# Optimization experiments

Measured on AMD Instinct MI355X. Metric: run time of the kernel, lower is better.

Reference implementation:

```python
import jax, jax.numpy as jnp
import numpy as np

EPS = 1e-6


def _conv(x, w, b=None, pad=0, groups=1):
    out = jax.lax.conv_general_dilated(
        x, w, window_strides=(1, 1), padding=[(pad, pad), (pad, pad)],
        feature_group_count=groups,
        dimension_numbers=("NCHW", "OIHW", "NCHW"))
    if b is not None:
        out = out + b[None, :, None, None]
    return out


def _win_patches(t):
    # t: [B, C, H, W] -> [B, C, 25, H, W]; 5x5 zero-padded sliding windows
    # (equivalent to torch nn.Unfold(5, padding=2), grouped per channel)
    B, C, H, W = t.shape
    p = jax.lax.conv_general_dilated_patches(
        t.reshape(B * C, 1, H, W), filter_shape=(5, 5),
        window_strides=(1, 1), padding=[(2, 2), (2, 2)])
    return p.reshape(B, C, 25, H, W)


def _gradient_consistency(gx, gy):
    mag = jnp.sqrt(gx * gx + gy * gy + EPS)
    direction = jnp.arctan2(gy, gx)
    dp = _win_patches(direction)          # [B,C,25,H,W]
    mp = _win_patches(mag)                # [B,C,25,H,W]
    sum_m = mp.sum(axis=2)                # [B,C,H,W]
    wmean = (dp * mp).sum(axis=2) / (sum_m + EPS)
    wvar = ((dp - wmean[:, :, None]) ** 2 * mp).sum(axis=2) / (sum_m + EPS)
    wstd = jnp.sqrt(wvar)
    return 1.0 - jnp.tanh(wstd)           # [B,C,H,W]


def setup_inputs() -> dict:
    key = jax.random.key(0)
    B, C, H, W = 2, 64, 128, 128
    C4 = C // 4
    ks = jax.random.split(key, 12)
    s = 0.02
    sobel_x = jnp.array([[-1, 0, 1], [-2, 0, 2], [-1, 0, 1]], jnp.float32)
    sobel_y = jnp.array([[-1, -2, -1], [0, 0, 0], [1, 2, 1]], jnp.float32)
    return {
        "x": jax.random.normal(ks[0], (B, C, H, W), jnp.float32),
        "w_gx": jnp.tile(sobel_x[None, None], (C, 1, 1, 1)),
        "w_gy": jnp.tile(sobel_y[None, None], (C, 1, 1, 1)),
        "ga_w1": jax.random.normal(ks[1], (C, 2 * C, 1, 1), jnp.float32) * s,
        "ga_b1": jnp.zeros((C,), jnp.float32),
        "ga_w2": jax.random.normal(ks[2], (C4, C, 1, 1), jnp.float32) * s,
        "ga_b2": jnp.zeros((C4,), jnp.float32),
        "cd_w1": jax.random.normal(ks[3], (C4, C4, 3, 3), jnp.float32) * s,
        "cd_b1": jnp.zeros((C4,), jnp.float32),
        "cd_w2": jax.random.normal(ks[4], (1, C4, 1, 1), jnp.float32) * s,
        "cd_b2": jnp.zeros((1,), jnp.float32),
        "ec_w1": jax.random.normal(ks[5], (C, C, 3, 3), jnp.float32) * s,
        "ec_b1": jnp.zeros((C,), jnp.float32),
        "ec_w2": jax.random.normal(ks[6], (C, C, 3, 3), jnp.float32) * s,
        "ec_b2": jnp.zeros((C,), jnp.float32),
        "alpha": jnp.float32(0.1),
    }


def reference(x, w_gx, w_gy, ga_w1, ga_b1, ga_w2, ga_b2,
              cd_w1, cd_b1, cd_w2, cd_b2,
              ec_w1, ec_b1, ec_w2, ec_b2, alpha):
    C = x.shape[1]
    # Sobel depthwise gradients
    gx = _conv(x, w_gx, pad=1, groups=C)
    gy = _conv(x, w_gy, pad=1, groups=C)
    # gradient analyzer (1x1 convs)
    gf = jnp.concatenate([gx, gy], axis=1)
    ga = jax.nn.relu(_conv(gf, ga_w1, ga_b1))
    ga = jax.nn.relu(_conv(ga, ga_w2, ga_b2))
    # windowed weighted direction stats
    consistency = _gradient_consistency(gx, gy)
    # consistency detector
    ew = jax.nn.relu(_conv(ga, cd_w1, cd_b1, pad=1))
    ew = jax.nn.sigmoid(_conv(ew, cd_w2, cd_b2))        # [B,1,H,W]
    ew = ew * consistency.mean(axis=1, keepdims=True)
    # edge branch
    ee = jax.nn.relu(_conv(x, ec_w1, ec_b1, pad=1))
    ee = _conv(ee, ec_w2, ec_b2, pad=1)
    return x + alpha * ew * ee
```

## Files before the change

kernel.cpp:

```cpp
#include <hip/hip_runtime.h>
#include <math.h>

#define Hd 128
#define Wd 128
#define HW 16384
#define EPSc 1e-6f

typedef __attribute__((ext_vector_type(8))) short s8v;
typedef __attribute__((ext_vector_type(4))) float f4v;

__device__ __forceinline__ unsigned short f2bf(float f) {
    unsigned int u = __float_as_uint(f);
    unsigned int r = (u + 0x7FFFu + ((u >> 16) & 1u)) >> 16;
    return (unsigned short)r;
}

__global__ void k_prepxh(const float* __restrict__ x,
                         const float* __restrict__ ga_w1, const float* __restrict__ ga_w2,
                         const float* __restrict__ cd_w1,
                         const float* __restrict__ ec_w1, const float* __restrict__ ec_w2,
                         unsigned short* __restrict__ xh,
                         unsigned short* __restrict__ w1m, unsigned short* __restrict__ w2m,
                         float* __restrict__ cd_w1t,
                         unsigned short* __restrict__ w1h, unsigned short* __restrict__ w2h,
                         float* __restrict__ cm) {
    int bid = blockIdx.x;
    if (bid < 128) {
        int p = bid * 256 + threadIdx.x;
        int b = p >> 14, s = p & (HW - 1);
        const float* xp = x + (size_t)b * 64 * HW + s;
        alignas(16) unsigned short buf[64];
#pragma unroll
        for (int c = 0; c < 64; c++) buf[c] = f2bf(xp[c * HW]);
        uint4* dst = (uint4*)(xh + (size_t)p * 64);
        const uint4* src = (const uint4*)buf;
#pragma unroll
        for (int i = 0; i < 8; i++) dst[i] = src[i];
        return;
    }
    int i = (bid - 128) * 256 + threadIdx.x;
    if (i < 36864) {
        int t = i >> 12, co = (i >> 6) & 63, ci = i & 63;
        w1h[i] = f2bf(ec_w1[(co * 64 + ci) * 9 + t]);
    } else if (i < 73728) {
        int j = i - 36864;
        int t = j >> 12, co = (j >> 6) & 63, ci = j & 63;
        w2h[j] = f2bf(ec_w2[(co * 64 + ci) * 9 + t]);
    } else if (i < 81920) {
        int j = i - 73728;
        w1m[j] = f2bf(ga_w1[j]);
    } else if (i < 82944) {
        int j = i - 81920;
        w2m[j] = f2bf(ga_w2[j]);
    } else if (i < 85248) {
        int j = i - 82944;
        int co = j & 15, r = j >> 4, t = r % 9, ci = r / 9;
        cd_w1t[j] = cd_w1[(co * 16 + ci) * 9 + t];
    } else if (i < 118016) {
        cm[i - 85248] = 0.f;
    }
}

__global__ __launch_bounds__(256, 8)
void k_sobcons(const float* __restrict__ x,
               const float* __restrict__ wgx, const float* __restrict__ wgy,
               unsigned short* __restrict__ gxgyh,
               float* __restrict__ cm) {
    __shared__ float xt[484];
    __shared__ float lm[480];
    __shared__ float ld[480];
    int tid = threadIdx.x;
    int tx = tid & 15, ty = tid >> 4;
    int x0 = blockIdx.x * 16, y0 = blockIdx.y * 16;
    int b = blockIdx.z >> 4, cb = (blockIdx.z & 15) * 4;
    float acc = 0.f;
    for (int c = 0; c < 4; c++) {
        int ch = cb + c;
        const float* xp = x + (size_t)(b * 64 + ch) * HW;
        float wx[9], wy[9];
#pragma unroll
        for (int i = 0; i < 9; i++) { wx[i] = wgx[ch * 9 + i]; wy[i] = wgy[ch * 9 + i]; }
        __syncthreads();
        for (int i = tid; i < 484; i += 256) {
            int yy = i / 22, xx = i - yy * 22;
            int gyy = y0 - 3 + yy, gxx = x0 - 3 + xx;
            xt[i] = (gyy >= 0 && gyy < Hd && gxx >= 0 && gxx < Wd) ? xp[gyy * Wd + gxx] : 0.f;
        }
        __syncthreads();
        for (int i = tid; i < 400; i += 256) {
            int yy = i / 20, xx = i - yy * 20;
            int gyy = y0 - 2 + yy, gxx = x0 - 2 + xx;
            float m = 0.f, d = 0.f, sx = 0.f, sy = 0.f;
            if (gyy >= 0 && gyy < Hd && gxx >= 0 && gxx < Wd) {
#pragma unroll
                for (int dy = 0; dy < 3; dy++)
#pragma unroll
                    for (int dx = 0; dx < 3; dx++) {
                        float v = xt[(yy + dy) * 22 + xx + dx];
                        sx = fmaf(wx[dy * 3 + dx], v, sx);
                        sy = fmaf(wy[dy * 3 + dx], v, sy);
                    }
                m = sqrtf(sx * sx + sy * sy + EPSc);
                d = atan2f(sy, sx);
            }
            lm[yy * 24 + xx] = m;
            ld[yy * 24 + xx] = d;
            if (yy >= 2 && yy < 18 && xx >= 2 && xx < 18) {
                size_t pb = ((size_t)b * HW + gyy * Wd + gxx) * 128;
                gxgyh[pb + ch] = f2bf(sx);
                gxgyh[pb + 64 + ch] = f2bf(sy);
            }
        }
        __syncthreads();
        float mv[25], dv[25];
        float sm = 0.f, sdm = 0.f;
#pragma unroll
        for (int r = 0; r < 5; r++)
#pragma unroll
            for (int cx = 0; cx < 5; cx++) {
                int idx = (ty + r) * 24 + tx + cx;
                float m = lm[idx], d = ld[idx];
                mv[r * 5 + cx] = m;
                dv[r * 5 + cx] = d;
                sm += m;
                sdm = fmaf(d, m, sdm);
            }
        float wmean = sdm / (sm + EPSc);
        float sv = 0.f;
#pragma unroll
        for (int t = 0; t < 25; t++) { float dd = dv[t] - wmean; sv = fmaf(dd * dd, mv[t], sv); }
        float wstd = sqrtf(sv / (sm + EPSc));
        acc += 1.f - tanhf(wstd);
    }
    atomicAdd(&cm[b * HW + (y0 + ty) * Wd + x0 + tx], acc * (1.f / 64.f));
}

__global__ __launch_bounds__(256, 2)
void k_gam(const unsigned short* __restrict__ gxgyh,
           const unsigned short* __restrict__ w1m, const float* __restrict__ b1,
           const unsigned short* __restrict__ w2m, const float* __restrict__ b2,
           float* __restrict__ ga2) {
    __shared__ unsigned short la[64 * 128];
    __shared__ unsigned short lp[64 * 64];
    int tid = threadIdx.x;
    int p0 = blockIdx.x * 64;
    int b = p0 >> 14;
    int s0 = p0 & (HW - 1);

    const unsigned short* src = gxgyh + (size_t)p0 * 128;
    for (int i = tid; i < 1024; i += 256) {
        int px = i >> 4, cg = i & 15;
        uint4 v = *(const uint4*)(src + px * 128 + cg * 8);
        *(uint4*)(la + px * 128 + ((cg ^ (px & 15)) * 8)) = v;
    }

    int lane = tid & 63, wv = tid >> 6;
    int l15 = lane & 15, lq = lane >> 4;
    int co_base = wv * 16;

    s8v af[4];
#pragma unroll
    for (int h = 0; h < 4; h++)
        af[h] = *(const s8v*)(w1m + (co_base + l15) * 128 + h * 32 + lq * 8);
    f4v bv = *(const f4v*)(b1 + co_base + lq * 4);
    f4v acc[4];
#pragma unroll
    for (int n = 0; n < 4; n++) acc[n] = bv;

    __syncthreads();

#pragma unroll
    for (int n = 0; n < 4; n++) {
        const unsigned short* tp = la + (n * 16 + l15) * 128;
#pragma unroll
        for (int h = 0; h < 4; h++) {
            s8v bb = *(const s8v*)(tp + (((h * 4 + lq) ^ l15) * 8));
            acc[n] = __builtin_amdgcn_mfma_f32_16x16x32_bf16(af[h], bb, acc[n], 0, 0, 0);
        }
    }

    int co = co_base + lq * 4;
    int og = co >> 3;
#pragma unroll
    for (int n = 0; n < 4; n++) {
        int px = n * 16 + l15;
        alignas(8) unsigned short pk[4];
#pragma unroll
        for (int r = 0; r < 4; r++) pk[r] = f2bf(fmaxf(acc[n][r], 0.f));
        *(uint2*)(lp + px * 64 + ((og ^ (px & 7)) * 8) + (co & 7)) = *(const uint2*)pk;
    }
    __syncthreads();

    s8v af2[2];
#pragma unroll
    for (int h = 0; h < 2; h++)
        af2[h] = *(const s8v*)(w2m + l15 * 64 + h * 32 + lq * 8);
    f4v acc2 = *(const f4v*)(b2 + lq * 4);
    int px2 = wv * 16 + l15;
    const unsigned short* tp2 = lp + px2 * 64;
#pragma unroll
    for (int h = 0; h < 2; h++) {
        s8v bb = *(const s8v*)(tp2 + (((h * 4 + lq) ^ (px2 & 7)) * 8));
        acc2 = __builtin_amdgcn_mfma_f32_16x16x32_bf16(af2[h], bb, acc2, 0, 0, 0);
    }
    float* op = ga2 + (size_t)b * 16 * HW + s0 + px2;
#pragma unroll
    for (int r = 0; r < 4; r++)
        op[(lq * 4 + r) * HW] = fmaxf(acc2[r], 0.f);
}

__global__ __launch_bounds__(256, 4)
void k_cd1ew(const float* __restrict__ ga2, const float* __restrict__ w1t,
             const float* __restrict__ b1, const float* __restrict__ w2,
             const float* __restrict__ b2, const float* __restrict__ cm,
             float* __restrict__ ew) {
    __shared__ float lds[16][324];
    int tid = threadIdx.x;
    int tx = tid & 15, ty = tid >> 4;
    int x0 = blockIdx.x * 16, y0 = blockIdx.y * 16;
    int b = blockIdx.z;
    const float* ip = ga2 + (size_t)b * 16 * HW;
    float acc[16];
#pragma unroll
    for (int co = 0; co < 16; co++) acc[co] = b1[co];
#pragma unroll
    for (int ci = 0; ci < 16; ci++) {
        const float* sp = ip + ci * HW;
        for (int i = tid; i < 324; i += 256) {
            int yy = i / 18, xx = i - yy * 18;
            int gy = y0 - 1 + yy, gx = x0 - 1 + xx;
            lds[ci][i] = (gy >= 0 && gy < Hd && gx >= 0 && gx < Wd) ? sp[gy * Wd + gx] : 0.f;
        }
    }
    __syncthreads();
    for (int ci = 0; ci < 16; ci++) {
        const float* wp = w1t + ci * 9 * 16;
        float pv[9];
#pragma unroll
        for (int r = 0; r < 3; r++)
#pragma unroll
            for (int cx = 0; cx < 3; cx++)
                pv[r * 3 + cx] = lds[ci][(ty + r) * 18 + tx + cx];
#pragma unroll
        for (int t = 0; t < 9; t++)
#pragma unroll
            for (int co = 0; co < 16; co++)
                acc[co] = fmaf(pv[t], wp[t * 16 + co], acc[co]);
    }
    float e = b2[0];
#pragma unroll
    for (int co = 0; co < 16; co++) e = fmaf(fmaxf(acc[co], 0.f), w2[co], e);
    float sig = 1.f / (1.f + expf(-e));
    int sp = (y0 + ty) * Wd + x0 + tx;
    ew[b * HW + sp] = sig * cm[b * HW + sp];
}

template <int FINAL>
__global__ __launch_bounds__(256, 2)
void k_conv64m(const unsigned short* __restrict__ inh,
               const unsigned short* __restrict__ wh,
               const float* __restrict__ bias,
               unsigned short* __restrict__ outh,
               float* __restrict__ outf,
               const float* __restrict__ x,
               const float* __restrict__ ew,
               const float* __restrict__ alpha_p) {
    __shared__ unsigned short tile[100 * 64];
    int tid = threadIdx.x;
    int x0 = blockIdx.x * 8, y0 = blockIdx.y * 8;
    int b = blockIdx.z;
    const size_t ibase = (size_t)b * HW * 64;

    for (int i = tid; i < 800; i += 256) {
        int py = i / 80;
        int r = i - py * 80;
        int px = r >> 3, cg = r & 7;
        int gy = y0 - 1 + py, gx = x0 - 1 + px;
        uint4 v = {0u, 0u, 0u, 0u};
        if (gy >= 0 && gy < Hd && gx >= 0 && gx < Wd)
            v = *(const uint4*)(inh + ibase + (size_t)(gy * Wd + gx) * 64 + cg * 8);
        int rowlin = py * 10 + px;
        int scg = cg ^ (rowlin & 7);
        *(uint4*)(tile + rowlin * 64 + scg * 8) = v;
    }

    int lane = tid & 63;
    int wv = tid >> 6;
    int l15 = lane & 15, lq = lane >> 4;
    int co_base = wv * 16;

    s8v af[9][2];
#pragma unroll
    for (int t = 0; t < 9; t++)
#pragma unroll
        for (int h = 0; h < 2; h++)
            af[t][h] = *(const s8v*)(wh + ((t * 64 + co_base + l15) * 64 + h * 32 + lq * 8));

    f4v bv = *(const f4v*)(bias + co_base + lq * 4);
    f4v acc[4];
#pragma unroll
    for (int n = 0; n < 4; n++) acc[n] = bv;

    __syncthreads();

#pragma unroll
    for (int n = 0; n < 4; n++) {
        int px = n * 16 + l15;
        int pyy = px >> 3, pxx = px & 7;
#pragma unroll
        for (int dy = 0; dy < 3; dy++) {
#pragma unroll
            for (int dx = 0; dx < 3; dx++) {
                int rowlin = (pyy + dy) * 10 + (pxx + dx);
                int sw = rowlin & 7;
                const unsigned short* tp = tile + rowlin * 64;
                s8v b0 = *(const s8v*)(tp + (lq ^ sw) * 8);
                s8v b1 = *(const s8v*)(tp + ((4 + lq) ^ sw) * 8);
                int t = dy * 3 + dx;
                acc[n] = __builtin_amdgcn_mfma_f32_16x16x32_bf16(af[t][0], b0, acc[n], 0, 0, 0);
                acc[n] = __builtin_amdgcn_mfma_f32_16x16x32_bf16(af[t][1], b1, acc[n], 0, 0, 0);
            }
        }
    }

#pragma unroll
    for (int n = 0; n < 4; n++) {
        int px = n * 16 + l15;
        int gyo = y0 + (px >> 3), gxo = x0 + (px & 7);
        int sp = gyo * Wd + gxo;
        if (FINAL) {
            float ae = alpha_p[0] * ew[b * HW + sp];
#pragma unroll
            for (int r = 0; r < 4; r++) {
                size_t o = (size_t)(b * 64 + co_base + lq * 4 + r) * HW + sp;
                outf[o] = fmaf(ae, acc[n][r], x[o]);
            }
        } else {
            alignas(8) unsigned short pk[4];
#pragma unroll
            for (int r = 0; r < 4; r++) pk[r] = f2bf(fmaxf(acc[n][r], 0.f));
            *(uint2*)(outh + ibase + (size_t)sp * 64 + co_base + lq * 4) = *(const uint2*)pk;
        }
    }
}

extern "C" void kernel_launch(void* const* d_in, const int* in_sizes, int n_in,
                              void* d_out, int out_size, void* d_ws, size_t ws_size,
                              hipStream_t stream) {
    const float* x     = (const float*)d_in[0];
    const float* wgx   = (const float*)d_in[1];
    const float* wgy   = (const float*)d_in[2];
    const float* ga_w1 = (const float*)d_in[3];
    const float* ga_b1 = (const float*)d_in[4];
    const float* ga_w2 = (const float*)d_in[5];
    const float* ga_b2 = (const float*)d_in[6];
    const float* cd_w1 = (const float*)d_in[7];
    const float* cd_b1 = (const float*)d_in[8];
    const float* cd_w2 = (const float*)d_in[9];
    const float* cd_b2 = (const float*)d_in[10];
    const float* ec_w1 = (const float*)d_in[11];
    const float* ec_b1 = (const float*)d_in[12];
    const float* ec_w2 = (const float*)d_in[13];
    const float* ec_b2 = (const float*)d_in[14];
    const float* alpha = (const float*)d_in[15];
    float* out = (float*)d_out;
    float* ws  = (float*)d_ws;

    const size_t N = 2 * 64 * HW;

    unsigned short* gxgyh = (unsigned short*)ws;
    float* ga2   = ws + N;
    float* cm    = ga2 + 2 * 16 * HW;
    float* ew    = cm + 2 * HW;
    float* cd_w1t = ew + 2 * HW;
    unsigned short* w1h = (unsigned short*)(cd_w1t + 2304);
    unsigned short* w2h = w1h + 36864;
    unsigned short* w1m = w2h + 36864;
    unsigned short* w2m = w1m + 8192;
    unsigned short* xh   = (unsigned short*)(ws + 2 * N);
    unsigned short* ee1h = xh + N;

    k_prepxh<<<590, 256, 0, stream>>>(x, ga_w1, ga_w2, cd_w1, ec_w1, ec_w2,
                                      xh, w1m, w2m, cd_w1t, w1h, w2h, cm);
    k_sobcons<<<dim3(8, 8, 32), 256, 0, stream>>>(x, wgx, wgy, gxgyh, cm);
    k_gam<<<512, 256, 0, stream>>>(gxgyh, w1m, ga_b1, w2m, ga_b2, ga2);
    k_cd1ew<<<dim3(8, 8, 2), 256, 0, stream>>>(ga2, cd_w1t, cd_b1, cd_w2, cd_b2, cm, ew);
    k_conv64m<0><<<dim3(16, 16, 2), 256, 0, stream>>>(xh, w1h, ec_b1, ee1h,
                                                      nullptr, nullptr, nullptr, nullptr);
    k_conv64m<1><<<dim3(16, 16, 2), 256, 0, stream>>>(ee1h, w2h, ec_b2, nullptr,
                                                      out, x, ew, alpha);
}
```

Before: 167.1 us.

## Merge independent stages into shared launches, replace atomics and use fast math

The prep and Sobel/consistency kernels are merged into one launch, and the first edge conv is merged with the gradient-analyzer kernel, cutting six launches to four and letting independent work share a grid. Per-channel-group partial consistency sums are written to separate buffers and reduced later in k_cd1ew. This replaces the atomicAdd and the zero-initialisation of cm. atan2, tanh, sigmoid and the divisions are replaced by a polynomial approximation, exp-based formulas and hardware reciprocals, which lowers accuracy slightly. The x-to-bf16 transpose is split across four channel groups for more parallelism.

```diff
diff --git a/kernel.cpp b/kernel.cpp
--- a/kernel.cpp
+++ b/kernel.cpp
@@ -15,30 +15,121 @@
     return (unsigned short)r;
 }
 
-__global__ void k_prepxh(const float* __restrict__ x,
-                         const float* __restrict__ ga_w1, const float* __restrict__ ga_w2,
-                         const float* __restrict__ cd_w1,
-                         const float* __restrict__ ec_w1, const float* __restrict__ ec_w2,
-                         unsigned short* __restrict__ xh,
-                         unsigned short* __restrict__ w1m, unsigned short* __restrict__ w2m,
-                         float* __restrict__ cd_w1t,
-                         unsigned short* __restrict__ w1h, unsigned short* __restrict__ w2h,
-                         float* __restrict__ cm) {
+__device__ __forceinline__ float rcpf(float x) { return __builtin_amdgcn_rcpf(x); }
+
+__device__ __forceinline__ float fatan2(float sy, float sx) {
+    float ax = fabsf(sx), ay = fabsf(sy);
+    float mx = fmaxf(ax, ay), mn = fminf(ax, ay);
+    float q = mn * rcpf(mx);
+    float s = q * q;
+    float r = q * fmaf(s, fmaf(s, fmaf(s, fmaf(s, 0.0208351f, -0.0851330f),
+                                       0.1801410f), -0.3302995f), 0.9998660f);
+    if (ay > ax) r = 1.5707963268f - r;
+    if (sx < 0.f) r = 3.14159265359f - r;
+    r = (sy < 0.f) ? -r : r;
+    return (mx == 0.f) ? 0.f : r;
+}
+
+__global__ __launch_bounds__(256, 8)
+void k_A(const float* __restrict__ x,
+         const float* __restrict__ wgx, const float* __restrict__ wgy,
+         const float* __restrict__ ga_w1, const float* __restrict__ ga_w2,
+         const float* __restrict__ cd_w1,
+         const float* __restrict__ ec_w1, const float* __restrict__ ec_w2,
+         unsigned short* __restrict__ gxgyh, float* __restrict__ cmPart,
+         unsigned short* __restrict__ xh,
+         unsigned short* __restrict__ w1m, unsigned short* __restrict__ w2m,
+         float* __restrict__ cd_w1t,
+         unsigned short* __restrict__ w1h, unsigned short* __restrict__ w2h) {
+    __shared__ float xt[484];
+    __shared__ float lm[480];
+    __shared__ float ld[480];
     int bid = blockIdx.x;
-    if (bid < 128) {
-        int p = bid * 256 + threadIdx.x;
+    int tid = threadIdx.x;
+
+    if (bid < 2048) {
+        int bx = bid & 7, by = (bid >> 3) & 7, z = bid >> 6;
+        int tx = tid & 15, ty = tid >> 4;
+        int x0 = bx * 16, y0 = by * 16;
+        int b = z >> 4, cb = (z & 15) * 4;
+        float acc = 0.f;
+        for (int c = 0; c < 4; c++) {
+            int ch = cb + c;
+            const float* xp = x + (size_t)(b * 64 + ch) * HW;
+            float wx[9], wy[9];
+#pragma unroll
+            for (int i = 0; i < 9; i++) { wx[i] = wgx[ch * 9 + i]; wy[i] = wgy[ch * 9 + i]; }
+            __syncthreads();
+            for (int i = tid; i < 484; i += 256) {
+                int yy = i / 22, xx = i - yy * 22;
+                int gyy = y0 - 3 + yy, gxx = x0 - 3 + xx;
+                xt[i] = (gyy >= 0 && gyy < Hd && gxx >= 0 && gxx < Wd) ? xp[gyy * Wd + gxx] : 0.f;
+            }
+            __syncthreads();
+            for (int i = tid; i < 400; i += 256) {
+                int yy = i / 20, xx = i - yy * 20;
+                int gyy = y0 - 2 + yy, gxx = x0 - 2 + xx;
+                float m = 0.f, d = 0.f, sx = 0.f, sy = 0.f;
+                if (gyy >= 0 && gyy < Hd && gxx >= 0 && gxx < Wd) {
+#pragma unroll
+                    for (int dy = 0; dy < 3; dy++)
+#pragma unroll
+                        for (int dx = 0; dx < 3; dx++) {
+                            float v = xt[(yy + dy) * 22 + xx + dx];
+                            sx = fmaf(wx[dy * 3 + dx], v, sx);
+                            sy = fmaf(wy[dy * 3 + dx], v, sy);
+                        }
+                    m = sqrtf(sx * sx + sy * sy + EPSc);
+                    d = fatan2(sy, sx);
+                }
+                lm[yy * 24 + xx] = m;
+                ld[yy * 24 + xx] = d;
+                if (yy >= 2 && yy < 18 && xx >= 2 && xx < 18) {
+                    size_t pb = ((size_t)b * HW + gyy * Wd + gxx) * 128;
+                    gxgyh[pb + ch] = f2bf(sx);
+                    gxgyh[pb + 64 + ch] = f2bf(sy);
+                }
+            }
+            __syncthreads();
+            float mv[25], dv[25];
+            float sm = 0.f, sdm = 0.f;
+#pragma unroll
+            for (int r = 0; r < 5; r++)
+#pragma unroll
+                for (int cx = 0; cx < 5; cx++) {
+                    int idx = (ty + r) * 24 + tx + cx;
+                    float m = lm[idx], d = ld[idx];
+                    mv[r * 5 + cx] = m;
+                    dv[r * 5 + cx] = d;
+                    sm += m;
+                    sdm = fmaf(d, m, sdm);
+                }
+            float rinv = rcpf(sm + EPSc);
+            float wmean = sdm * rinv;
+            float sv = 0.f;
+#pragma unroll
+            for (int t = 0; t < 25; t++) { float dd = dv[t] - wmean; sv = fmaf(dd * dd, mv[t], sv); }
+            float wstd = sqrtf(sv * rinv);
+            acc += 2.f * rcpf(__expf(2.f * wstd) + 1.f);
+        }
+        cmPart[(size_t)z * HW + (y0 + ty) * Wd + x0 + tx] = acc * (1.f / 64.f);
+        return;
+    }
+    if (bid < 2560) {
+        int idx = (bid - 2048) * 256 + tid;
+        int cg = idx >> 15;
+        int p  = idx & 32767;
         int b = p >> 14, s = p & (HW - 1);
-        const float* xp = x + (size_t)b * 64 * HW + s;
-        alignas(16) unsigned short buf[64];
-#pragma unroll
-        for (int c = 0; c < 64; c++) buf[c] = f2bf(xp[c * HW]);
-        uint4* dst = (uint4*)(xh + (size_t)p * 64);
-        const uint4* src = (const uint4*)buf;
-#pragma unroll
-        for (int i = 0; i < 8; i++) dst[i] = src[i];
+        const float* xp = x + ((size_t)b * 64 + cg * 16) * HW + s;
+        alignas(16) unsigned short buf[16];
+#pragma unroll
+        for (int k = 0; k < 16; k++) buf[k] = f2bf(xp[k * HW]);
+        uint4* dst = (uint4*)(xh + (size_t)p * 64 + cg * 16);
+        dst[0] = ((const uint4*)buf)[0];
+        dst[1] = ((const uint4*)buf)[1];
         return;
     }
-    int i = (bid - 128) * 256 + threadIdx.x;
+    int i = (bid - 2560) * 256 + tid;
     if (i < 36864) {
         int t = i >> 12, co = (i >> 6) & 63, ci = i & 63;
         w1h[i] = f2bf(ec_w1[(co * 64 + ci) * 9 + t]);
@@ -56,94 +147,88 @@
         int j = i - 82944;
         int co = j & 15, r = j >> 4, t = r % 9, ci = r / 9;
         cd_w1t[j] = cd_w1[(co * 16 + ci) * 9 + t];
-    } else if (i < 118016) {
-        cm[i - 85248] = 0.f;
-    }
-}
-
-__global__ __launch_bounds__(256, 8)
-void k_sobcons(const float* __restrict__ x,
-               const float* __restrict__ wgx, const float* __restrict__ wgy,
-               unsigned short* __restrict__ gxgyh,
-               float* __restrict__ cm) {
-    __shared__ float xt[484];
-    __shared__ float lm[480];
-    __shared__ float ld[480];
+    }
+}
+
+__global__ __launch_bounds__(256, 2)
+void k_B(const unsigned short* __restrict__ xh,
+         const unsigned short* __restrict__ w1h, const float* __restrict__ ec_b1,
+         unsigned short* __restrict__ ee1h,
+         const unsigned short* __restrict__ gxgyh,
+         const unsigned short* __restrict__ w1m, const float* __restrict__ b1,
+         const unsigned short* __restrict__ w2m, const float* __restrict__ b2,
+         float* __restrict__ ga2) {
+    __shared__ unsigned short shb[12288];
+    int bid = blockIdx.x;
     int tid = threadIdx.x;
-    int tx = tid & 15, ty = tid >> 4;
-    int x0 = blockIdx.x * 16, y0 = blockIdx.y * 16;
-    int b = blockIdx.z >> 4, cb = (blockIdx.z & 15) * 4;
-    float acc = 0.f;
-    for (int c = 0; c < 4; c++) {
-        int ch = cb + c;
-        const float* xp = x + (size_t)(b * 64 + ch) * HW;
-        float wx[9], wy[9];
-#pragma unroll
-        for (int i = 0; i < 9; i++) { wx[i] = wgx[ch * 9 + i]; wy[i] = wgy[ch * 9 + i]; }
+    int lane = tid & 63, wv = tid >> 6;
+    int l15 = lane & 15, lq = lane >> 4;
+
+    if (bid < 512) {
+        unsigned short* tile = shb;
+        int j = bid;
+        int x0 = (j & 15) * 8, y0 = ((j >> 4) & 15) * 8;
+        int b = j >> 8;
+        const size_t ibase = (size_t)b * HW * 64;
+
+        for (int i = tid; i < 800; i += 256) {
+            int py = i / 80;
+            int r = i - py * 80;
+            int px = r >> 3, cg = r & 7;
+            int gy = y0 - 1 + py, gx = x0 - 1 + px;
+            uint4 v = {0u, 0u, 0u, 0u};
+            if (gy >= 0 && gy < Hd && gx >= 0 && gx < Wd)
+                v = *(const uint4*)(xh + ibase + (size_t)(gy * Wd + gx) * 64 + cg * 8);
+            int rowlin = py * 10 + px;
+            int scg = cg ^ (rowlin & 7);
+            *(uint4*)(tile + rowlin * 64 + scg * 8) = v;
+        }
+        int co_base = wv * 16;
+        s8v af[9][2];
+#pragma unroll
+        for (int t = 0; t < 9; t++)
+#pragma unroll
+            for (int h = 0; h < 2; h++)
+                af[t][h] = *(const s8v*)(w1h + ((t * 64 + co_base + l15) * 64 + h * 32 + lq * 8));
+        f4v bv = *(const f4v*)(ec_b1 + co_base + lq * 4);
+        f4v acc[4];
+#pragma unroll
+        for (int n = 0; n < 4; n++) acc[n] = bv;
         __syncthreads();
-        for (int i = tid; i < 484; i += 256) {
-            int yy = i / 22, xx = i - yy * 22;
-            int gyy = y0 - 3 + yy, gxx = x0 - 3 + xx;
-            xt[i] = (gyy >= 0 && gyy < Hd && gxx >= 0 && gxx < Wd) ? xp[gyy * Wd + gxx] : 0.f;
-        }
-        __syncthreads();
-        for (int i = tid; i < 400; i += 256) {
-            int yy = i / 20, xx = i - yy * 20;
-            int gyy = y0 - 2 + yy, gxx = x0 - 2 + xx;
-            float m = 0.f, d = 0.f, sx = 0.f, sy = 0.f;
-            if (gyy >= 0 && gyy < Hd && gxx >= 0 && gxx < Wd) {
-#pragma unroll
-                for (int dy = 0; dy < 3; dy++)
-#pragma unroll
-                    for (int dx = 0; dx < 3; dx++) {
-                        float v = xt[(yy + dy) * 22 + xx + dx];
-                        sx = fmaf(wx[dy * 3 + dx], v, sx);
-                        sy = fmaf(wy[dy * 3 + dx], v, sy);
-                    }
-                m = sqrtf(sx * sx + sy * sy + EPSc);
-                d = atan2f(sy, sx);
+#pragma unroll
+        for (int n = 0; n < 4; n++) {
+            int px = n * 16 + l15;
+            int pyy = px >> 3, pxx = px & 7;
+#pragma unroll
+            for (int dy = 0; dy < 3; dy++) {
+#pragma unroll
+                for (int dx = 0; dx < 3; dx++) {
+                    int rowlin = (pyy + dy) * 10 + (pxx + dx);
+                    int sw = rowlin & 7;
+                    const unsigned short* tp = tile + rowlin * 64;
+                    s8v b0 = *(const s8v*)(tp + (lq ^ sw) * 8);
+                    s8v b1v = *(const s8v*)(tp + ((4 + lq) ^ sw) * 8);
+                    int t = dy * 3 + dx;
+                    acc[n] = __builtin_amdgcn_mfma_f32_16x16x32_bf16(af[t][0], b0, acc[n], 0, 0, 0);
+                    acc[n] = __builtin_amdgcn_mfma_f32_16x16x32_bf16(af[t][1], b1v, acc[n], 0, 0, 0);
+                }
             }
-            lm[yy * 24 + xx] = m;
-            ld[yy * 24 + xx] = d;
-            if (yy >= 2 && yy < 18 && xx >= 2 && xx < 18) {
-                size_t pb = ((size_t)b * HW + gyy * Wd + gxx) * 128;
-                gxgyh[pb + ch] = f2bf(sx);
-                gxgyh[pb + 64 + ch] = f2bf(sy);
-            }
-        }
-        __syncthreads();
-        float mv[25], dv[25];
-        float sm = 0.f, sdm = 0.f;
-#pragma unroll
-        for (int r = 0; r < 5; r++)
-#pragma unroll
-            for (int cx = 0; cx < 5; cx++) {
-                int idx = (ty + r) * 24 + tx + cx;
-                float m = lm[idx], d = ld[idx];
-                mv[r * 5 + cx] = m;
-                dv[r * 5 + cx] = d;
-                sm += m;
-                sdm = fmaf(d, m, sdm);
-            }
-        float wmean = sdm / (sm + EPSc);
-        float sv = 0.f;
-#pragma unroll
-        for (int t = 0; t < 25; t++) { float dd = dv[t] - wmean; sv = fmaf(dd * dd, mv[t], sv); }
-        float wstd = sqrtf(sv / (sm + EPSc));
-        acc += 1.f - tanhf(wstd);
-    }
-    atomicAdd(&cm[b * HW + (y0 + ty) * Wd + x0 + tx], acc * (1.f / 64.f));
-}
-
-__global__ __launch_bounds__(256, 2)
-void k_gam(const unsigned short* __restrict__ gxgyh,
-           const unsigned short* __restrict__ w1m, const float* __restrict__ b1,
-           const unsigned short* __restrict__ w2m, const float* __restrict__ b2,
-           float* __restrict__ ga2) {
-    __shared__ unsigned short la[64 * 128];
-    __shared__ unsigned short lp[64 * 64];
-    int tid = threadIdx.x;
-    int p0 = blockIdx.x * 64;
+        }
+#pragma unroll
+        for (int n = 0; n < 4; n++) {
+            int px = n * 16 + l15;
+            int sp = (y0 + (px >> 3)) * Wd + x0 + (px & 7);
+            alignas(8) unsigned short pk[4];
+#pragma unroll
+            for (int r = 0; r < 4; r++) pk[r] = f2bf(fmaxf(acc[n][r], 0.f));
+            *(uint2*)(ee1h + ibase + (size_t)sp * 64 + co_base + lq * 4) = *(const uint2*)pk;
+        }
+        return;
+    }
+
+    unsigned short* la = shb;
+    unsigned short* lp = shb + 8192;
+    int p0 = (bid - 512) * 64;
     int b = p0 >> 14;
     int s0 = p0 & (HW - 1);
 
@@ -153,11 +238,7 @@
         uint4 v = *(const uint4*)(src + px * 128 + cg * 8);
         *(uint4*)(la + px * 128 + ((cg ^ (px & 15)) * 8)) = v;
     }
-
-    int lane = tid & 63, wv = tid >> 6;
-    int l15 = lane & 15, lq = lane >> 4;
     int co_base = wv * 16;
-
     s8v af[4];
 #pragma unroll
     for (int h = 0; h < 4; h++)
@@ -166,9 +247,7 @@
     f4v acc[4];
 #pragma unroll
     for (int n = 0; n < 4; n++) acc[n] = bv;
-
     __syncthreads();
-
 #pragma unroll
     for (int n = 0; n < 4; n++) {
         const unsigned short* tp = la + (n * 16 + l15) * 128;
@@ -178,7 +257,6 @@
             acc[n] = __builtin_amdgcn_mfma_f32_16x16x32_bf16(af[h], bb, acc[n], 0, 0, 0);
         }
     }
-
     int co = co_base + lq * 4;
     int og = co >> 3;
 #pragma unroll
@@ -190,7 +268,6 @@
         *(uint2*)(lp + px * 64 + ((og ^ (px & 7)) * 8) + (co & 7)) = *(const uint2*)pk;
     }
     __syncthreads();
-
     s8v af2[2];
 #pragma unroll
     for (int h = 0; h < 2; h++)
@@ -212,7 +289,7 @@
 __global__ __launch_bounds__(256, 4)
 void k_cd1ew(const float* __restrict__ ga2, const float* __restrict__ w1t,
              const float* __restrict__ b1, const float* __restrict__ w2,
-             const float* __restrict__ b2, const float* __restrict__ cm,
+             const float* __restrict__ b2, const float* __restrict__ cmPart,
              float* __restrict__ ew) {
     __shared__ float lds[16][324];
     int tid = threadIdx.x;
@@ -250,17 +327,18 @@
     float e = b2[0];
 #pragma unroll
     for (int co = 0; co < 16; co++) e = fmaf(fmaxf(acc[co], 0.f), w2[co], e);
-    float sig = 1.f / (1.f + expf(-e));
+    float sig = rcpf(1.f + __expf(-e));
     int sp = (y0 + ty) * Wd + x0 + tx;
-    ew[b * HW + sp] = sig * cm[b * HW + sp];
-}
-
-template <int FINAL>
+    float cmv = 0.f;
+#pragma unroll
+    for (int q = 0; q < 16; q++) cmv += cmPart[(size_t)((b << 4) + q) * HW + sp];
+    ew[b * HW + sp] = sig * cmv;
+}
+
 __global__ __launch_bounds__(256, 2)
-void k_conv64m(const unsigned short* __restrict__ inh,
+void k_conv64f(const unsigned short* __restrict__ inh,
                const unsigned short* __restrict__ wh,
                const float* __restrict__ bias,
-               unsigned short* __restrict__ outh,
                float* __restrict__ outf,
                const float* __restrict__ x,
                const float* __restrict__ ew,
@@ -283,26 +361,21 @@
         int scg = cg ^ (rowlin & 7);
         *(uint4*)(tile + rowlin * 64 + scg * 8) = v;
     }
-
     int lane = tid & 63;
     int wv = tid >> 6;
     int l15 = lane & 15, lq = lane >> 4;
     int co_base = wv * 16;
-
     s8v af[9][2];
 #pragma unroll
     for (int t = 0; t < 9; t++)
 #pragma unroll
         for (int h = 0; h < 2; h++)
             af[t][h] = *(const s8v*)(wh + ((t * 64 + co_base + l15) * 64 + h * 32 + lq * 8));
-
     f4v bv = *(const f4v*)(bias + co_base + lq * 4);
     f4v acc[4];
 #pragma unroll
     for (int n = 0; n < 4; n++) acc[n] = bv;
-
     __syncthreads();
-
 #pragma unroll
     for (int n = 0; n < 4; n++) {
         int px = n * 16 + l15;
@@ -315,31 +388,22 @@
                 int sw = rowlin & 7;
                 const unsigned short* tp = tile + rowlin * 64;
                 s8v b0 = *(const s8v*)(tp + (lq ^ sw) * 8);
-                s8v b1 = *(const s8v*)(tp + ((4 + lq) ^ sw) * 8);
+                s8v b1v = *(const s8v*)(tp + ((4 + lq) ^ sw) * 8);
                 int t = dy * 3 + dx;
                 acc[n] = __builtin_amdgcn_mfma_f32_16x16x32_bf16(af[t][0], b0, acc[n], 0, 0, 0);
-                acc[n] = __builtin_amdgcn_mfma_f32_16x16x32_bf16(af[t][1], b1, acc[n], 0, 0, 0);
+                acc[n] = __builtin_amdgcn_mfma_f32_16x16x32_bf16(af[t][1], b1v, acc[n], 0, 0, 0);
             }
         }
     }
-
 #pragma unroll
     for (int n = 0; n < 4; n++) {
         int px = n * 16 + l15;
-        int gyo = y0 + (px >> 3), gxo = x0 + (px & 7);
-        int sp = gyo * Wd + gxo;
-        if (FINAL) {
-            float ae = alpha_p[0] * ew[b * HW + sp];
-#pragma unroll
-            for (int r = 0; r < 4; r++) {
-                size_t o = (size_t)(b * 64 + co_base + lq * 4 + r) * HW + sp;
-                outf[o] = fmaf(ae, acc[n][r], x[o]);
-            }
-        } else {
-            alignas(8) unsigned short pk[4];
-#pragma unroll
-            for (int r = 0; r < 4; r++) pk[r] = f2bf(fmaxf(acc[n][r], 0.f));
-            *(uint2*)(outh + ibase + (size_t)sp * 64 + co_base + lq * 4) = *(const uint2*)pk;
+        int sp = (y0 + (px >> 3)) * Wd + x0 + (px & 7);
+        float ae = alpha_p[0] * ew[b * HW + sp];
+#pragma unroll
+        for (int r = 0; r < 4; r++) {
+            size_t o = (size_t)(b * 64 + co_base + lq * 4 + r) * HW + sp;
+            outf[o] = fmaf(ae, acc[n][r], x[o]);
         }
     }
 }
@@ -369,9 +433,9 @@
     const size_t N = 2 * 64 * HW;
 
     unsigned short* gxgyh = (unsigned short*)ws;
-    float* ga2   = ws + N;
-    float* cm    = ga2 + 2 * 16 * HW;
-    float* ew    = cm + 2 * HW;
+    float* ga2    = ws + N;
+    float* cmPart = ga2 + 2 * 16 * HW;
+    float* ew     = cmPart + 32 * HW;
     float* cd_w1t = ew + 2 * HW;
     unsigned short* w1h = (unsigned short*)(cd_w1t + 2304);
     unsigned short* w2h = w1h + 36864;
@@ -380,13 +444,11 @@
     unsigned short* xh   = (unsigned short*)(ws + 2 * N);
     unsigned short* ee1h = xh + N;
 
-    k_prepxh<<<590, 256, 0, stream>>>(x, ga_w1, ga_w2, cd_w1, ec_w1, ec_w2,
-                                      xh, w1m, w2m, cd_w1t, w1h, w2h, cm);
-    k_sobcons<<<dim3(8, 8, 32), 256, 0, stream>>>(x, wgx, wgy, gxgyh, cm);
-    k_gam<<<512, 256, 0, stream>>>(gxgyh, w1m, ga_b1, w2m, ga_b2, ga2);
-    k_cd1ew<<<dim3(8, 8, 2), 256, 0, stream>>>(ga2, cd_w1t, cd_b1, cd_w2, cd_b2, cm, ew);
-    k_conv64m<0><<<dim3(16, 16, 2), 256, 0, stream>>>(xh, w1h, ec_b1, ee1h,
-                                                      nullptr, nullptr, nullptr, nullptr);
-    k_conv64m<1><<<dim3(16, 16, 2), 256, 0, stream>>>(ee1h, w2h, ec_b2, nullptr,
-                                                      out, x, ew, alpha);
-}
+    k_A<<<2893, 256, 0, stream>>>(x, wgx, wgy, ga_w1, ga_w2, cd_w1, ec_w1, ec_w2,
+                                  gxgyh, cmPart, xh, w1m, w2m, cd_w1t, w1h, w2h);
+    k_B<<<1024, 256, 0, stream>>>(xh, w1h, ec_b1, ee1h,
+                                  gxgyh, w1m, ga_b1, w2m, ga_b2, ga2);
+    k_cd1ew<<<dim3(8, 8, 2), 256, 0, stream>>>(ga2, cd_w1t, cd_b1, cd_w2, cd_b2,
+                                               cmPart, ew);
+    k_conv64f<<<dim3(16, 16, 2), 256, 0, stream>>>(ee1h, w2h, ec_b2, out, x, ew, alpha);
+}
```

Result: faster. 158.0 us (-5.4%).
